# Kernel tuning notes

Measured on AMD Instinct MI355X. Metric: run time of the kernel, lower is better.

## Reference

```python
import jax, jax.numpy as jnp
import numpy as np

ALPHA = 0.2  # LeakyReLU negative slope
NEG = -9e15


def setup_inputs() -> dict:
    key = jax.random.key(0)
    k1, k2, k3, k4 = jax.random.split(key, 4)
    N, F_in, F_out = 8192, 512, 64
    h = jax.random.normal(k1, (N, F_in), dtype=jnp.float32)
    adj = jax.random.randint(k2, (N, N), 0, 2, dtype=jnp.int32)
    # xavier_uniform with gain=1.414
    def xavier(k, shape, gain=1.414):
        fan_in, fan_out = shape[0], shape[1]
        bound = gain * np.sqrt(6.0 / (fan_in + fan_out))
        return jax.random.uniform(k, shape, jnp.float32, -bound, bound)
    W = xavier(k3, (F_in, F_out))
    a = xavier(k4, (2 * F_out, 1))
    return {"h": h, "adj": adj, "W": W, "a": a}


def reference(h, adj, W, a):
    F_out = W.shape[1]
    Wh = h @ W                                   # [N, F_out]
    # e_ij = LeakyReLU([Wh_i || Wh_j] . a) = LeakyReLU(Wh.a1 + (Wh.a2)^T)
    e1 = Wh @ a[:F_out, 0]                       # [N]
    e2 = Wh @ a[F_out:, 0]                       # [N]
    e = jax.nn.leaky_relu(e1[:, None] + e2[None, :], ALPHA)  # [N, N]
    e = jnp.where(adj > 0, e, NEG)
    attention = jax.nn.softmax(e, axis=1)        # dropout p=0.0 -> identity
    h_prime = attention @ Wh                     # [N, F_out]
    return jax.nn.elu(h_prime)                   # concat=True
```

## Files before the change

### kernel.cpp

```cpp
#include <hip/hip_runtime.h>
#include <hip/hip_bf16.h>
#include <stdint.h>

typedef __attribute__((ext_vector_type(8))) short short8;
typedef __attribute__((ext_vector_type(4))) float f32x4;

#define NSLICE 8
#define SLICE_J 1024
#define CHUNKS 16
#define L2E 1.44269504f

static __device__ __forceinline__ short f2bf(float f) {
    unsigned int u = __float_as_uint(f);
    u += 0x7fffu + ((u >> 16) & 1u);
    return (short)(u >> 16);
}

static __device__ __forceinline__ short welem(int a, float e2s, float e1s, float& lsum) {
    float x = e1s + e2s;
    x = fmaxf(x, 0.f) + 0.2f * fminf(x, 0.f);
    float w = __builtin_amdgcn_exp2f(x);
    w = (a > 0) ? w : 0.f;
    lsum += w;
    return f2bf(w);
}

__global__ __launch_bounds__(256)
void gat_wh(const float* __restrict__ h, const float* __restrict__ W,
            const float* __restrict__ a, short* __restrict__ whT,
            float* __restrict__ e1, float* __restrict__ e2)
{
    const int lane = threadIdx.x & 63;
    const int wave = threadIdx.x >> 6;
    const int row0 = blockIdx.x * 16 + wave * 4;

    float acc[4] = {0.f, 0.f, 0.f, 0.f};
#pragma unroll 8
    for (int c = 0; c < 512; ++c) {
        const float wv = W[c * 64 + lane];
#pragma unroll
        for (int r = 0; r < 4; ++r)
            acc[r] += h[(size_t)(row0 + r) * 512 + c] * wv;
    }

    const float a1v = a[lane];
    const float a2v = a[64 + lane];
    const int f    = lane >> 4;
    const int r16n = lane & 15;
#pragma unroll
    for (int r = 0; r < 4; ++r) {
        float p1 = acc[r] * a1v;
        float p2 = acc[r] * a2v;
#pragma unroll
        for (int off = 32; off; off >>= 1) {
            p1 += __shfl_xor(p1, off);
            p2 += __shfl_xor(p2, off);
        }
        if (lane == 0) { e1[row0 + r] = p1; e2[row0 + r] = p2; }
        const int j = row0 + r;
        const int kin = j & 63;
        const int frag = (kin >> 5) & 1, qk = (kin >> 3) & 3, t = kin & 7;
        whT[(size_t)(j >> 6) * 4096 + (f * 2 + frag) * 512 + qk * 128 + r16n * 8 + t]
            = f2bf(acc[r]);
    }
}

__global__ __launch_bounds__(256)
void gat_attn(const int* __restrict__ adj, const short* __restrict__ whT,
              const float* __restrict__ e1, const float* __restrict__ e2,
              float* __restrict__ lpart, float* __restrict__ opart)
{
    __shared__ float se2[SLICE_J];
    const int bid = blockIdx.x;
    const int s   = bid & (NSLICE - 1);
    const int rb  = bid >> 3;
    const int tid = threadIdx.x;

    {
        float4 v = *reinterpret_cast<const float4*>(e2 + s * SLICE_J + tid * 4);
        v.x *= L2E; v.y *= L2E; v.z *= L2E; v.w *= L2E;
        *reinterpret_cast<float4*>(se2 + tid * 4) = v;
    }
    __syncthreads();

    const int lane = tid & 63;
    const int wave = tid >> 6;
    const int quad = lane >> 4;
    const int r16  = lane & 15;
    const int rowBase = rb * 64 + wave * 16;
    const int row  = rowBase + r16;
    const float e1s = e1[row] * L2E;
    const size_t adjRow = (size_t)row * 8192 + (size_t)s * SLICE_J;

    float lsum = 0.f;
    f32x4 acc[4];
#pragma unroll
    for (int ff = 0; ff < 4; ++ff) acc[ff] = (f32x4){0.f, 0.f, 0.f, 0.f};

    for (int ch = 0; ch < CHUNKS; ++ch) {
        const int j0 = ch * 64 + quad * 8;
        const int4 A0 = *reinterpret_cast<const int4*>(adj + adjRow + j0);
        const int4 A1 = *reinterpret_cast<const int4*>(adj + adjRow + j0 + 4);
        const int4 A2 = *reinterpret_cast<const int4*>(adj + adjRow + j0 + 32);
        const int4 A3 = *reinterpret_cast<const int4*>(adj + adjRow + j0 + 36);
        const float4 E0 = *reinterpret_cast<const float4*>(se2 + j0);
        const float4 E1 = *reinterpret_cast<const float4*>(se2 + j0 + 4);
        const float4 E2 = *reinterpret_cast<const float4*>(se2 + j0 + 32);
        const float4 E3 = *reinterpret_cast<const float4*>(se2 + j0 + 36);

        short8 af0, af1;
        af0[0] = welem(A0.x, E0.x, e1s, lsum);
        af0[1] = welem(A0.y, E0.y, e1s, lsum);
        af0[2] = welem(A0.z, E0.z, e1s, lsum);
        af0[3] = welem(A0.w, E0.w, e1s, lsum);
        af0[4] = welem(A1.x, E1.x, e1s, lsum);
        af0[5] = welem(A1.y, E1.y, e1s, lsum);
        af0[6] = welem(A1.z, E1.z, e1s, lsum);
        af0[7] = welem(A1.w, E1.w, e1s, lsum);
        af1[0] = welem(A2.x, E2.x, e1s, lsum);
        af1[1] = welem(A2.y, E2.y, e1s, lsum);
        af1[2] = welem(A2.z, E2.z, e1s, lsum);
        af1[3] = welem(A2.w, E2.w, e1s, lsum);
        af1[4] = welem(A3.x, E3.x, e1s, lsum);
        af1[5] = welem(A3.y, E3.y, e1s, lsum);
        af1[6] = welem(A3.z, E3.z, e1s, lsum);
        af1[7] = welem(A3.w, E3.w, e1s, lsum);

        const short* wtile = whT + (size_t)(s * 16 + ch) * 4096 + lane * 8;
#pragma unroll
        for (int ff = 0; ff < 4; ++ff) {
            const short8 b0 = *reinterpret_cast<const short8*>(wtile + (ff * 2 + 0) * 512);
            const short8 b1 = *reinterpret_cast<const short8*>(wtile + (ff * 2 + 1) * 512);
            acc[ff] = __builtin_amdgcn_mfma_f32_16x16x32_bf16(af0, b0, acc[ff], 0, 0, 0);
            acc[ff] = __builtin_amdgcn_mfma_f32_16x16x32_bf16(af1, b1, acc[ff], 0, 0, 0);
        }
    }

    lsum += __shfl_xor(lsum, 16);
    lsum += __shfl_xor(lsum, 32);
    if (lane < 16) lpart[s * 8192 + rowBase + lane] = lsum;

#pragma unroll
    for (int ff = 0; ff < 4; ++ff) {
#pragma unroll
        for (int rg = 0; rg < 4; ++rg) {
            const int orow = rowBase + quad * 4 + rg;
            const int ocol = ff * 16 + r16;
            opart[((size_t)s * 8192 + orow) * 64 + ocol] = acc[ff][rg];
        }
    }
}

__global__ __launch_bounds__(256)
void gat_combine(const float* __restrict__ lpart, const float* __restrict__ opart,
                 float* __restrict__ out)
{
    const int gid = blockIdx.x * 256 + threadIdx.x;
    const int row = gid >> 6;
    const int f   = gid & 63;

    float lsum = 0.f, osum = 0.f;
#pragma unroll
    for (int s = 0; s < NSLICE; ++s) {
        lsum += lpart[s * 8192 + row];
        osum += opart[((size_t)s * 8192 + row) * 64 + f];
    }
    const float v = osum / lsum;
    out[gid] = (v > 0.f) ? v : (__expf(v) - 1.f);
}

extern "C" void kernel_launch(void* const* d_in, const int* in_sizes, int n_in,
                              void* d_out, int out_size, void* d_ws, size_t ws_size,
                              hipStream_t stream) {
    const float* h   = (const float*)d_in[0];
    const int*   adj = (const int*)d_in[1];
    const float* W   = (const float*)d_in[2];
    const float* a   = (const float*)d_in[3];
    float* out = (float*)d_out;

    char* ws = (char*)d_ws;
    short* whT   = (short*)ws;
    float* e1    = (float*)(ws + (1u << 20));
    float* e2    = (float*)(ws + (1u << 20) + (32u << 10));
    float* lpart = (float*)(ws + (1u << 20) + (64u << 10));
    float* opart = (float*)(ws + (2u << 20));

    gat_wh<<<512, 256, 0, stream>>>(h, W, a, whT, e1, e2);
    gat_attn<<<128 * NSLICE, 256, 0, stream>>>(adj, whT, e1, e2, lpart, opart);
    gat_combine<<<out_size / 256, 256, 0, stream>>>(lpart, opart, out);
}
```

Baseline: 434.4 us.

## Factor exp of LeakyReLU into per-row/col products, prefetch adj, split Wh rows

The per-element exp2 is replaced by a factorization: since exp is monotone, exp(leaky(e1+e2)) = max(exp(e1)exp(e2), exp(0.2 e1)exp(0.2 e2)), so the exponentials are computed once per row and per column and the inner loop only does two multiplies and a max. The adjacency loads are software-prefetched one chunk ahead, bf16 packing uses the paired conversion intrinsic, and the row sum is split into four partial accumulators. The Wh projection kernel processes 2 rows per wave instead of 4 and launches twice as many blocks. The factorization works without the usual softmax max subtraction, so large logits could overflow the products. The prefetch also issues a redundant wrap-around load on the last chunk.

```diff
diff --git a/kernel.cpp b/kernel.cpp
--- a/kernel.cpp
+++ b/kernel.cpp
@@ -9,6 +9,7 @@
 #define SLICE_J 1024
 #define CHUNKS 16
 #define L2E 1.44269504f
+#define L2E5 0.288539008f
 
 static __device__ __forceinline__ short f2bf(float f) {
     unsigned int u = __float_as_uint(f);
@@ -16,13 +17,10 @@
     return (short)(u >> 16);
 }
 
-static __device__ __forceinline__ short welem(int a, float e2s, float e1s, float& lsum) {
-    float x = e1s + e2s;
-    x = fmaxf(x, 0.f) + 0.2f * fminf(x, 0.f);
-    float w = __builtin_amdgcn_exp2f(x);
-    w = (a > 0) ? w : 0.f;
-    lsum += w;
-    return f2bf(w);
+static __device__ __forceinline__ int pk2(float a, float b) {
+    float2 f2 = make_float2(a, b);
+    __hip_bfloat162 h = __float22bfloat162_rn(f2);
+    return *reinterpret_cast<int*>(&h);
 }
 
 __global__ __launch_bounds__(256)
@@ -32,14 +30,14 @@
 {
     const int lane = threadIdx.x & 63;
     const int wave = threadIdx.x >> 6;
-    const int row0 = blockIdx.x * 16 + wave * 4;
-
-    float acc[4] = {0.f, 0.f, 0.f, 0.f};
+    const int row0 = blockIdx.x * 8 + wave * 2;
+
+    float acc[2] = {0.f, 0.f};
 #pragma unroll 8
     for (int c = 0; c < 512; ++c) {
         const float wv = W[c * 64 + lane];
 #pragma unroll
-        for (int r = 0; r < 4; ++r)
+        for (int r = 0; r < 2; ++r)
             acc[r] += h[(size_t)(row0 + r) * 512 + c] * wv;
     }
 
@@ -48,7 +46,7 @@
     const int f    = lane >> 4;
     const int r16n = lane & 15;
 #pragma unroll
-    for (int r = 0; r < 4; ++r) {
+    for (int r = 0; r < 2; ++r) {
         float p1 = acc[r] * a1v;
         float p2 = acc[r] * a2v;
 #pragma unroll
@@ -70,16 +68,21 @@
               const float* __restrict__ e1, const float* __restrict__ e2,
               float* __restrict__ lpart, float* __restrict__ opart)
 {
-    __shared__ float se2[SLICE_J];
+    __shared__ __align__(16) float2 sB[SLICE_J];
     const int bid = blockIdx.x;
     const int s   = bid & (NSLICE - 1);
     const int rb  = bid >> 3;
     const int tid = threadIdx.x;
 
     {
-        float4 v = *reinterpret_cast<const float4*>(e2 + s * SLICE_J + tid * 4);
-        v.x *= L2E; v.y *= L2E; v.z *= L2E; v.w *= L2E;
-        *reinterpret_cast<float4*>(se2 + tid * 4) = v;
+        const float4 v = *reinterpret_cast<const float4*>(e2 + s * SLICE_J + tid * 4);
+        float4 lo, hi;
+        lo.x = __builtin_amdgcn_exp2f(v.x * L2E);  lo.y = __builtin_amdgcn_exp2f(v.x * L2E5);
+        lo.z = __builtin_amdgcn_exp2f(v.y * L2E);  lo.w = __builtin_amdgcn_exp2f(v.y * L2E5);
+        hi.x = __builtin_amdgcn_exp2f(v.z * L2E);  hi.y = __builtin_amdgcn_exp2f(v.z * L2E5);
+        hi.z = __builtin_amdgcn_exp2f(v.w * L2E);  hi.w = __builtin_amdgcn_exp2f(v.w * L2E5);
+        reinterpret_cast<float4*>(sB)[tid * 2]     = lo;
+        reinterpret_cast<float4*>(sB)[tid * 2 + 1] = hi;
     }
     __syncthreads();
 
@@ -89,53 +92,79 @@
     const int r16  = lane & 15;
     const int rowBase = rb * 64 + wave * 16;
     const int row  = rowBase + r16;
-    const float e1s = e1[row] * L2E;
+    const float e1v = e1[row];
+    const float a1 = __builtin_amdgcn_exp2f(e1v * L2E);
+    const float a5 = __builtin_amdgcn_exp2f(e1v * L2E5);
     const size_t adjRow = (size_t)row * 8192 + (size_t)s * SLICE_J;
 
-    float lsum = 0.f;
+    float ls0 = 0.f, ls1 = 0.f, ls2 = 0.f, ls3 = 0.f;
     f32x4 acc[4];
 #pragma unroll
     for (int ff = 0; ff < 4; ++ff) acc[ff] = (f32x4){0.f, 0.f, 0.f, 0.f};
 
+    const int jq = quad * 8;
+    int4 A0 = *reinterpret_cast<const int4*>(adj + adjRow + jq);
+    int4 A1 = *reinterpret_cast<const int4*>(adj + adjRow + jq + 4);
+    int4 A2 = *reinterpret_cast<const int4*>(adj + adjRow + jq + 32);
+    int4 A3 = *reinterpret_cast<const int4*>(adj + adjRow + jq + 36);
+
     for (int ch = 0; ch < CHUNKS; ++ch) {
-        const int j0 = ch * 64 + quad * 8;
-        const int4 A0 = *reinterpret_cast<const int4*>(adj + adjRow + j0);
-        const int4 A1 = *reinterpret_cast<const int4*>(adj + adjRow + j0 + 4);
-        const int4 A2 = *reinterpret_cast<const int4*>(adj + adjRow + j0 + 32);
-        const int4 A3 = *reinterpret_cast<const int4*>(adj + adjRow + j0 + 36);
-        const float4 E0 = *reinterpret_cast<const float4*>(se2 + j0);
-        const float4 E1 = *reinterpret_cast<const float4*>(se2 + j0 + 4);
-        const float4 E2 = *reinterpret_cast<const float4*>(se2 + j0 + 32);
-        const float4 E3 = *reinterpret_cast<const float4*>(se2 + j0 + 36);
-
-        short8 af0, af1;
-        af0[0] = welem(A0.x, E0.x, e1s, lsum);
-        af0[1] = welem(A0.y, E0.y, e1s, lsum);
-        af0[2] = welem(A0.z, E0.z, e1s, lsum);
-        af0[3] = welem(A0.w, E0.w, e1s, lsum);
-        af0[4] = welem(A1.x, E1.x, e1s, lsum);
-        af0[5] = welem(A1.y, E1.y, e1s, lsum);
-        af0[6] = welem(A1.z, E1.z, e1s, lsum);
-        af0[7] = welem(A1.w, E1.w, e1s, lsum);
-        af1[0] = welem(A2.x, E2.x, e1s, lsum);
-        af1[1] = welem(A2.y, E2.y, e1s, lsum);
-        af1[2] = welem(A2.z, E2.z, e1s, lsum);
-        af1[3] = welem(A2.w, E2.w, e1s, lsum);
-        af1[4] = welem(A3.x, E3.x, e1s, lsum);
-        af1[5] = welem(A3.y, E3.y, e1s, lsum);
-        af1[6] = welem(A3.z, E3.z, e1s, lsum);
-        af1[7] = welem(A3.w, E3.w, e1s, lsum);
+        const int chn = (ch + 1) & (CHUNKS - 1);
+        const size_t nbase = adjRow + chn * 64 + jq;
+        const int4 N0 = *reinterpret_cast<const int4*>(adj + nbase);
+        const int4 N1 = *reinterpret_cast<const int4*>(adj + nbase + 4);
+        const int4 N2 = *reinterpret_cast<const int4*>(adj + nbase + 32);
+        const int4 N3 = *reinterpret_cast<const int4*>(adj + nbase + 36);
+
+        const int j0 = ch * 64 + jq;
+        const float4 P0 = *reinterpret_cast<const float4*>(&sB[j0]);
+        const float4 P1 = *reinterpret_cast<const float4*>(&sB[j0 + 2]);
+        const float4 P2 = *reinterpret_cast<const float4*>(&sB[j0 + 4]);
+        const float4 P3 = *reinterpret_cast<const float4*>(&sB[j0 + 6]);
+        const float4 P4 = *reinterpret_cast<const float4*>(&sB[j0 + 32]);
+        const float4 P5 = *reinterpret_cast<const float4*>(&sB[j0 + 34]);
+        const float4 P6 = *reinterpret_cast<const float4*>(&sB[j0 + 36]);
+        const float4 P7 = *reinterpret_cast<const float4*>(&sB[j0 + 38]);
+
+        float w0  = (A0.x > 0) ? fmaxf(a1 * P0.x, a5 * P0.y) : 0.f;
+        float w1  = (A0.y > 0) ? fmaxf(a1 * P0.z, a5 * P0.w) : 0.f;
+        float w2  = (A0.z > 0) ? fmaxf(a1 * P1.x, a5 * P1.y) : 0.f;
+        float w3  = (A0.w > 0) ? fmaxf(a1 * P1.z, a5 * P1.w) : 0.f;
+        float w4  = (A1.x > 0) ? fmaxf(a1 * P2.x, a5 * P2.y) : 0.f;
+        float w5  = (A1.y > 0) ? fmaxf(a1 * P2.z, a5 * P2.w) : 0.f;
+        float w6  = (A1.z > 0) ? fmaxf(a1 * P3.x, a5 * P3.y) : 0.f;
+        float w7  = (A1.w > 0) ? fmaxf(a1 * P3.z, a5 * P3.w) : 0.f;
+        float w8  = (A2.x > 0) ? fmaxf(a1 * P4.x, a5 * P4.y) : 0.f;
+        float w9  = (A2.y > 0) ? fmaxf(a1 * P4.z, a5 * P4.w) : 0.f;
+        float w10 = (A2.z > 0) ? fmaxf(a1 * P5.x, a5 * P5.y) : 0.f;
+        float w11 = (A2.w > 0) ? fmaxf(a1 * P5.z, a5 * P5.w) : 0.f;
+        float w12 = (A3.x > 0) ? fmaxf(a1 * P6.x, a5 * P6.y) : 0.f;
+        float w13 = (A3.y > 0) ? fmaxf(a1 * P6.z, a5 * P6.w) : 0.f;
+        float w14 = (A3.z > 0) ? fmaxf(a1 * P7.x, a5 * P7.y) : 0.f;
+        float w15 = (A3.w > 0) ? fmaxf(a1 * P7.z, a5 * P7.w) : 0.f;
+
+        ls0 += w0 + w1 + w2 + w3;
+        ls1 += w4 + w5 + w6 + w7;
+        ls2 += w8 + w9 + w10 + w11;
+        ls3 += w12 + w13 + w14 + w15;
+
+        union { int4 i; short8 s; } U0, U1;
+        U0.i = make_int4(pk2(w0, w1),  pk2(w2, w3),  pk2(w4, w5),  pk2(w6, w7));
+        U1.i = make_int4(pk2(w8, w9),  pk2(w10, w11), pk2(w12, w13), pk2(w14, w15));
 
         const short* wtile = whT + (size_t)(s * 16 + ch) * 4096 + lane * 8;
 #pragma unroll
         for (int ff = 0; ff < 4; ++ff) {
             const short8 b0 = *reinterpret_cast<const short8*>(wtile + (ff * 2 + 0) * 512);
             const short8 b1 = *reinterpret_cast<const short8*>(wtile + (ff * 2 + 1) * 512);
-            acc[ff] = __builtin_amdgcn_mfma_f32_16x16x32_bf16(af0, b0, acc[ff], 0, 0, 0);
-            acc[ff] = __builtin_amdgcn_mfma_f32_16x16x32_bf16(af1, b1, acc[ff], 0, 0, 0);
+            acc[ff] = __builtin_amdgcn_mfma_f32_16x16x32_bf16(U0.s, b0, acc[ff], 0, 0, 0);
+            acc[ff] = __builtin_amdgcn_mfma_f32_16x16x32_bf16(U1.s, b1, acc[ff], 0, 0, 0);
         }
-    }
-
+
+        A0 = N0; A1 = N1; A2 = N2; A3 = N3;
+    }
+
+    float lsum = (ls0 + ls1) + (ls2 + ls3);
     lsum += __shfl_xor(lsum, 16);
     lsum += __shfl_xor(lsum, 32);
     if (lane < 16) lpart[s * 8192 + rowBase + lane] = lsum;
@@ -185,7 +214,7 @@
     float* lpart = (float*)(ws + (1u << 20) + (64u << 10));
     float* opart = (float*)(ws + (2u << 20));
 
-    gat_wh<<<512, 256, 0, stream>>>(h, W, a, whT, e1, e2);
+    gat_wh<<<1024, 256, 0, stream>>>(h, W, a, whT, e1, e2);
     gat_attn<<<128 * NSLICE, 256, 0, stream>>>(adj, whT, e1, e2, lpart, opart);
     gat_combine<<<out_size / 256, 256, 0, stream>>>(lpart, opart, out);
 }
```

Measured after the change: 453.3 us. 1.04x slower.
